# Kernel tuning notes

Hardware: AMD Instinct MI355X
Metric: run time of the kernel (lower is better)

The kernel has to match this reference:

```python
import math
import jax, jax.numpy as jnp
import numpy as np

NUM_HEADS = 8
EMBED_DIM = 512   # embed_dim_per_head(64) * num_heads(8)
LATENT = 256
HIDDEN = 512
INPUT_DIM = 128
P = 3             # function 'Q' -> 3 polynomial coefficients


def setup_inputs() -> dict:
    key = jax.random.key(0)
    ks = jax.random.split(key, 16)
    B, L, T, D, E = 64, 2048, 1024, INPUT_DIM, EMBED_DIM
    s = lambda fan_in: 1.0 / math.sqrt(fan_in)
    inp = {
        "timesteps": jax.random.uniform(ks[0], (B, L), jnp.float32),
        "X": jax.random.normal(ks[1], (B, L, D), jnp.float32),
        "M": jax.random.bernoulli(ks[2], 0.5, (B, L, D)).astype(jnp.float32),
        "y_time_steps": jax.random.uniform(ks[3], (B, T), jnp.float32),
        # time_embedding: Linear(1, E)
        "w_te": jax.random.normal(ks[4], (E,), jnp.float32),
        "b_te": jnp.zeros((E,), jnp.float32),
        # learned query [1, P, E]
        "query": jax.random.normal(ks[5], (1, P, E), jnp.float32),
        # query_map / key_map: Linear(E, E), stored [in, out]
        "W_q": jax.random.normal(ks[6], (E, E), jnp.float32) * s(E),
        "b_q": jnp.zeros((E,), jnp.float32),
        "W_k": jax.random.normal(ks[7], (E, E), jnp.float32) * s(E),
        "b_k": jnp.zeros((E,), jnp.float32),
        # attn out: Linear(2*D*H, latent)
        "W_o": jax.random.normal(ks[8], (2 * D * NUM_HEADS, LATENT), jnp.float32) * s(2 * D * NUM_HEADS),
        "b_o": jnp.zeros((LATENT,), jnp.float32),
        # decoder MLP: latent -> hidden -> hidden -> D
        "W1": jax.random.normal(ks[9], (LATENT, HIDDEN), jnp.float32) * s(LATENT),
        "b1": jnp.zeros((HIDDEN,), jnp.float32),
        "W2": jax.random.normal(ks[10], (HIDDEN, HIDDEN), jnp.float32) * s(HIDDEN),
        "b2": jnp.zeros((HIDDEN,), jnp.float32),
        "W3": jax.random.normal(ks[11], (HIDDEN, D), jnp.float32) * s(HIDDEN),
        "b3": jnp.zeros((D,), jnp.float32),
    }
    return inp


def _fld_forward(timesteps, X, M, y_time_steps, w_te, b_te, query,
                 W_q, b_q, W_k, b_k, W_o, b_o, W1, b1, W2, b2, W3, b3):
    B, L = timesteps.shape
    D = X.shape[-1]
    E, H = EMBED_DIM, NUM_HEADS
    ek = E // H
    # learn_time_embedding: Linear(1,E) then sin on indices range(0, E, H)
    key = timesteps[..., None] * w_te + b_te                      # [B,L,E]
    sin_mask = (jnp.arange(E) % H) == 0
    key = jnp.where(sin_mask, jnp.sin(key), key)
    Xcat = jnp.concatenate([X, M], axis=-1)                       # [B,L,2D]
    Mcat = jnp.concatenate([M, M], axis=-1)                       # [B,L,2D]
    # mask is used only for masked_fill in torch (no grad through it)
    maskb = jax.lax.stop_gradient((Mcat != 0).astype(Xcat.dtype))
    q = jnp.broadcast_to(query, (B, P, E)) @ W_q + b_q            # [B,P,E]
    k = key @ W_k + b_k                                            # [B,L,E]
    qh = q.reshape(B, P, H, ek).transpose(0, 2, 1, 3)             # [B,H,P,ek]
    kh = k.reshape(B, L, H, ek).transpose(0, 2, 1, 3)             # [B,H,L,ek]
    scores = jnp.einsum('bhpe,bhle->bhpl', qh, kh) / math.sqrt(ek)
    # per-channel masked softmax over L, factorized (masked entries -> exp(-1e9)=0)
    m = jnp.max(scores, axis=-1, keepdims=True)
    w = jnp.exp(scores - m)                                        # [B,H,P,L]
    num = jnp.einsum('bhpl,blc->bhpc', w, maskb * Xcat)            # [B,H,P,2D]
    den = jnp.einsum('bhpl,blc->bhpc', w, maskb)
    x = num / den                                                  # [B,H,P,2D]
    x = x.transpose(0, 2, 1, 3).reshape(B, P, H * 2 * D)
    coeffs = x @ W_o + b_o                                         # [B,P,latent]
    t = y_time_steps[..., None]                                    # [B,T,1]
    c0 = coeffs[:, 0:1, :]
    c1 = coeffs[:, 1:2, :]
    c2 = coeffs[:, 2:3, :]
    z = c0 + t * c1 + (t * t) * c2                                 # [B,T,latent]
    h1 = jax.nn.relu(z @ W1 + b1)
    h2 = jax.nn.relu(h1 @ W2 + b2)
    return h2 @ W3 + b3                                            # [B,T,D]


def reference(timesteps, X, M, y_time_steps, w_te, b_te, query,
              W_q, b_q, W_k, b_k, W_o, b_o, W1, b1, W2, b2, W3, b3):
    return _fld_forward(timesteps, X, M, y_time_steps, w_te, b_te, query,
                        W_q, b_q, W_k, b_k, W_o, b_o, W1, b1, W2, b2, W3, b3)
```

## Files before the change

### kernel.cpp

```cpp
#include <hip/hip_runtime.h>
#include <math.h>

#define NH   8
#define PP   3
#define HP   24
#define E    512
#define EK   64
#define D    128
#define LL   2048
#define BB   64
#define TT   1024
#define LAT  256
#define HID  512
#define CH   8
#define CL   256

typedef __attribute__((ext_vector_type(8))) short bf16x8;
typedef __attribute__((ext_vector_type(4))) float f32x4;
typedef __attribute__((ext_vector_type(16))) float f32x16;

#define OFF_VS     ((size_t)2048)
#define OFF_WA     ((size_t)4096)
#define OFF_WB     ((size_t)4128)
#define OFF_SB     ((size_t)4160)
#define OFF_CVP    ((size_t)73728)
#define OFF_P2     ((size_t)81920)
#define OFF_PART   ((size_t)475136)
#define OFF_SC     ((size_t)3620864)
#define OFF_A      ((size_t)3784704)

__device__ inline ushort f2bf(float x) {
    union { float f; uint u; } v; v.f = x;
    uint r = v.u + 0x7fffu + ((v.u >> 16) & 1u);
    return (ushort)(r >> 16);
}
__device__ inline uint swz(uint a)  { return a ^ (((a >> 8) & 7u) << 4); }
__device__ inline uint swzH(uint a) { return a ^ (((a >> 7) & 7u) << 4); }
__device__ inline uint swzQ(uint a) { return a ^ (((a >> 9) & 7u) << 4); }
__device__ inline uint pk2(float lo, float hi) {
    return (uint)f2bf(lo) | ((uint)f2bf(hi) << 16);
}
__device__ inline float h1f(float a0, float a1, float a2, float t) {
    return fmaxf(fmaf(t, fmaf(t, a2, a1), a0), 0.f);
}
__device__ inline int sigma(int s) { return s ^ (((((s >> 2) ^ (s >> 3)) & 1)) ? 12 : 0); }

__global__ __launch_bounds__(512) void k_setup(const float* __restrict__ query,
                                               const float* __restrict__ W_q,
                                               const float* __restrict__ b_q,
                                               const float* __restrict__ W_k,
                                               const float* __restrict__ b_k,
                                               const float* __restrict__ w_te,
                                               const float* __restrict__ b_te,
                                               const float* __restrict__ W_o,
                                               float* __restrict__ vsin,
                                               float* __restrict__ wA,
                                               float* __restrict__ wB,
                                               float* __restrict__ sbias,
                                               float* __restrict__ cvp) {
    int bx = blockIdx.x, tid = threadIdx.x;
    if (bx < HP) {
        int hp = bx, h = hp / PP, p = hp % PP;
        __shared__ float q_s[EK];
        if (tid < EK) {
            float acc = b_q[h * EK + tid];
            for (int i = 0; i < E; ++i)
                acc += query[p * E + i] * W_q[(size_t)i * E + h * EK + tid];
            q_s[tid] = acc;
        }
        __syncthreads();
        int e = tid;
        const float scale = 0.125f;
        float acc = 0.f;
        for (int j = 0; j < EK; ++j)
            acc += W_k[(size_t)e * E + h * EK + j] * q_s[j];
        float v = acc * scale;
        if ((e & 7) == 0) vsin[hp * 64 + (e >> 3)] = v;
        __shared__ float r1[512], r2[512];
        r1[e] = v * w_te[e];
        r2[e] = v * b_te[e];
        __syncthreads();
        for (int s = 256; s > 0; s >>= 1) {
            if (e < s) { r1[e] += r1[e + s]; r2[e] += r2[e + s]; }
            __syncthreads();
        }
        if (e == 0) {
            wA[hp] = r1[0];
            wB[hp] = r2[0];
            float sb = 0.f;
            for (int j = 0; j < EK; ++j) sb += b_k[h * EK + j] * q_s[j];
            sbias[hp] = sb * scale;
        }
    } else {
        int bc = bx - HP;
        int h = bc >> 2, cc = bc & 3, o = tid & 255;
        float acc = 0.f;
        #pragma unroll 8
        for (int c = cc * 32; c < cc * 32 + 32; ++c)
            acc += W_o[(size_t)(h * 256 + 128 + c) * LAT + o];
        cvp[(h * 4 + cc) * LAT + o] = acc;
    }
}

__global__ __launch_bounds__(512) void k_wsf(const float* __restrict__ timesteps,
                                             const float* __restrict__ w_te,
                                             const float* __restrict__ b_te,
                                             const float* __restrict__ vsin,
                                             const float* __restrict__ wA,
                                             const float* __restrict__ wB,
                                             const float* __restrict__ sb,
                                             const float* __restrict__ X,
                                             const float* __restrict__ M,
                                             float* __restrict__ part) {
    __shared__ float vs_s[HP * 64];
    __shared__ float w8_s[64], b8_s[64];
    __shared__ float wA_s[HP], wB_s[HP], sb_s[HP];
    __shared__ ushort w_s[32 * 256];
    __shared__ ushort vt[256 * 64];
    int b = blockIdx.x / CH, ch = blockIdx.x % CH;
    int l0 = ch * CL;
    int tid = threadIdx.x;

    for (int i = tid; i < HP * 64; i += 512) vs_s[i] = vsin[i];
    if (tid < 64) { w8_s[tid] = w_te[tid * 8]; b8_s[tid] = b_te[tid * 8]; }
    if (tid < HP) { wA_s[tid] = wA[tid]; wB_s[tid] = wB[tid]; sb_s[tid] = sb[tid]; }
    __syncthreads();

    {
        int lpair = tid & 127, hh = tid >> 7;
        float ts0 = timesteps[(size_t)b * LL + l0 + lpair * 2];
        float ts1 = timesteps[(size_t)b * LL + l0 + lpair * 2 + 1];
        float sc0[6], sc1[6];
        #pragma unroll
        for (int i = 0; i < 6; ++i) {
            int hp = hh * 6 + i;
            sc0[i] = fmaf(ts0, wA_s[hp], wB_s[hp]) + sb_s[hp];
            sc1[i] = fmaf(ts1, wA_s[hp], wB_s[hp]) + sb_s[hp];
        }
        for (int jc = 0; jc < 64; jc += 16) {
            float d0[16], d1[16];
            #pragma unroll
            for (int j = 0; j < 16; ++j) {
                float w = w8_s[jc + j], bb = b8_s[jc + j];
                float k0 = fmaf(ts0, w, bb), k1 = fmaf(ts1, w, bb);
                d0[j] = __sinf(k0) - k0;
                d1[j] = __sinf(k1) - k1;
            }
            #pragma unroll
            for (int i = 0; i < 6; ++i) {
                int hp = hh * 6 + i;
                #pragma unroll
                for (int j = 0; j < 16; j += 4) {
                    float4 v4 = *(const float4*)&vs_s[hp * 64 + jc + j];
                    sc0[i] += d0[j] * v4.x + d0[j+1] * v4.y + d0[j+2] * v4.z + d0[j+3] * v4.w;
                    sc1[i] += d1[j] * v4.x + d1[j+1] * v4.y + d1[j+2] * v4.z + d1[j+3] * v4.w;
                }
            }
        }
        #pragma unroll
        for (int i = 0; i < 6; ++i) {
            int hp = hh * 6 + i;
            *(uint*)((char*)w_s + swzQ((uint)(hp * 512 + lpair * 4))) = pk2(__expf(sc0[i]), __expf(sc1[i]));
        }
        for (int idx = tid; idx < 8 * 128; idx += 512) {
            int hp = 24 + (idx >> 7), lp = idx & 127;
            *(uint*)((char*)w_s + swzQ((uint)(hp * 512 + lp * 4))) = 0u;
        }
    }

    int lane = tid & 63, wv = tid >> 6;
    int l31 = lane & 31, hl = lane >> 5;
    f32x16 acc;
    #pragma unroll
    for (int e = 0; e < 16; ++e) acc[e] = 0.f;

    int cst = tid & 127, lg = tid >> 7;
    for (int q = 0; q < 4; ++q) {
        if (q) __syncthreads();
        #pragma unroll
        for (int i = 0; i < 8; ++i) {
            int ll = lg * 16 + i * 2;
            size_t g0 = ((size_t)b * LL + l0 + q * 64 + ll) * D + cst;
            float m0 = M[g0], m1 = M[g0 + D];
            float x0 = X[g0] * m0, x1 = X[g0 + D] * m1;
            *(uint*)((char*)vt + swzH((uint)(cst * 128 + ll * 2)))         = pk2(x0, x1);
            *(uint*)((char*)vt + swzH((uint)((128 + cst) * 128 + ll * 2))) = pk2(m0, m1);
        }
        __syncthreads();
        #pragma unroll
        for (int ks = 0; ks < 4; ++ks) {
            bf16x8 af = *(const bf16x8*)((char*)w_s + swzQ((uint)(l31 * 512 + (q * 64 + ks * 16 + hl * 8) * 2)));
            bf16x8 bf_ = *(const bf16x8*)((char*)vt + swzH((uint)((wv * 32 + l31) * 128 + (ks * 16 + hl * 8) * 2)));
            acc = __builtin_amdgcn_mfma_f32_32x32x16_bf16(af, bf_, acc, 0, 0, 0);
        }
    }
    size_t base = ((size_t)(b * CH + ch) * HP) * 256;
    #pragma unroll
    for (int reg = 0; reg < 12; ++reg) {
        int hp = (reg & 3) + 8 * (reg >> 2) + 4 * hl;
        part[base + (size_t)hp * 256 + wv * 32 + l31] = acc[reg];
    }
}

__global__ __launch_bounds__(512) void k_mid(const float* __restrict__ part,
                                             const float* __restrict__ W_o,
                                             float* __restrict__ part2,
                                             const float* __restrict__ W2,
                                             const float* __restrict__ W3,
                                             ushort* __restrict__ W2F,
                                             ushort* __restrict__ W3F) {
    int bx = blockIdx.x, tid = threadIdx.x;
    if (bx < BB * NH) {
        int b = bx >> 3, h = bx & 7, t = tid & 255;
        __shared__ float ratio[PP][D];
        for (int ii = t; ii < PP * D; ii += 256) {
            int p = ii >> 7, c = ii & 127;
            int hp = h * PP + p;
            float n = 0.f, d = 0.f;
            for (int ch = 0; ch < CH; ++ch) {
                size_t base = ((size_t)(b * CH + ch) * HP + hp) * 256;
                n += part[base + c];
                d += part[base + 128 + c];
            }
            ratio[p][c] = n / d;
        }
        __syncthreads();
        int o = t;
        float a0 = 0.f, a1 = 0.f, a2 = 0.f;
        #pragma unroll 4
        for (int c = 0; c < D; ++c) {
            float w = W_o[(size_t)(h * 256 + c) * LAT + o];
            a0 = fmaf(ratio[0][c], w, a0);
            a1 = fmaf(ratio[1][c], w, a1);
            a2 = fmaf(ratio[2][c], w, a2);
        }
        size_t base = (((size_t)b * NH + h) * PP) * LAT + o;
        part2[base]           = a0;
        part2[base + LAT]     = a1;
        part2[base + 2 * LAT] = a2;
    } else {
        int gid = (bx - BB * NH) * 512 + tid;
        int l = gid & 63;
        int kb = 8 * (l >> 5);
        int cb = l & 31;
        if (gid < 32768) {
            int F = gid >> 6;
            int JT = F & 15, ks = F >> 4;
            int cbp = sigma(cb);
            int k0 = ks * 16 + kb, j = JT * 32 + cbp;
            #pragma unroll
            for (int e = 0; e < 8; ++e)
                W2F[(size_t)gid * 8 + e] = f2bf(W2[(size_t)(k0 + e) * HID + j]);
        } else {
            int g2 = gid - 32768;
            int F2 = g2 >> 6;
            int CT = F2 & 3, KT = F2 >> 2;
            int k0 = KT * 16 + kb, c = CT * 32 + cb;
            #pragma unroll
            for (int e = 0; e < 8; ++e)
                W3F[(size_t)g2 * 8 + e] = f2bf(W3[(size_t)(k0 + e) * D + c]);
        }
    }
}

__global__ __launch_bounds__(512) void k_avec3p(const float* __restrict__ part2,
                                                const float* __restrict__ cvp,
                                                const float* __restrict__ b_o,
                                                const float* __restrict__ W1,
                                                const float* __restrict__ b1,
                                                float* __restrict__ abuf) {
    int b = blockIdx.x, tid = threadIdx.x;
    __shared__ float cf[PP * LAT];
    for (int idx = tid; idx < PP * LAT; idx += 512) {
        int p = idx / LAT, o = idx % LAT;
        float s = b_o[o];
        #pragma unroll 8
        for (int i = 0; i < 32; ++i) s += cvp[i * LAT + o];
        for (int h = 0; h < NH; ++h)
            s += part2[(((size_t)b * NH + h) * PP + p) * LAT + o];
        cf[p * LAT + o] = s;
    }
    __syncthreads();
    int j = tid;
    float a0 = b1[j], a1 = 0.f, a2 = 0.f;
    #pragma unroll 4
    for (int k = 0; k < LAT; ++k) {
        float w = W1[(size_t)k * HID + j];
        a0 = fmaf(cf[k], w, a0);
        a1 = fmaf(cf[LAT + k], w, a1);
        a2 = fmaf(cf[2 * LAT + k], w, a2);
    }
    abuf[(size_t)b * 3 * HID + j] = a0;
    abuf[(size_t)b * 3 * HID + HID + j] = a1;
    abuf[(size_t)b * 3 * HID + 2 * HID + j] = a2;
}

__global__ __launch_bounds__(512, 2) void k_mlp13(const float* __restrict__ abuf,
                                                  const float* __restrict__ yts,
                                                  const ushort* __restrict__ W2F,
                                                  const float* __restrict__ b2,
                                                  const ushort* __restrict__ W3F,
                                                  const float* __restrict__ b3,
                                                  float* __restrict__ out) {
    __shared__ char lds[65536];
    int b = blockIdx.x, t0 = blockIdx.y * 64, tid = threadIdx.x;
    const float* a0p = abuf + (size_t)b * 3 * HID;
    const float* a1p = a0p + HID;
    const float* a2p = a1p + HID;

    {
        int sr = tid & 63, sub0 = (tid >> 6) & 1, skp = tid >> 7;
        float t = yts[(size_t)b * TT + t0 + sr];
        int kg0 = skp * 128 + sub0 * 64;
        uint sbase = (uint)(skp * 16384 + sr * 256 + sub0 * 128);
        #pragma unroll
        for (int i = 0; i < 8; ++i) {
            int k = kg0 + i * 8;
            float4 xa0 = *(const float4*)(a0p + k), xb0 = *(const float4*)(a0p + k + 4);
            float4 xa1 = *(const float4*)(a1p + k), xb1 = *(const float4*)(a1p + k + 4);
            float4 xa2 = *(const float4*)(a2p + k), xb2 = *(const float4*)(a2p + k + 4);
            uint4 pk;
            pk.x = pk2(h1f(xa0.x, xa1.x, xa2.x, t), h1f(xa0.y, xa1.y, xa2.y, t));
            pk.y = pk2(h1f(xa0.z, xa1.z, xa2.z, t), h1f(xa0.w, xa1.w, xa2.w, t));
            pk.z = pk2(h1f(xb0.x, xb1.x, xb2.x, t), h1f(xb0.y, xb1.y, xb2.y, t));
            pk.w = pk2(h1f(xb0.z, xb1.z, xb2.z, t), h1f(xb0.w, xb1.w, xb2.w, t));
            *(uint4*)(lds + swz(sbase + i * 16)) = pk;
        }
    }
    __syncthreads();

    int lane = tid & 63, w = tid >> 6;
    int l31 = lane & 31, hl = lane >> 5;
    int wp = w & 1, gw = w >> 1;
    int Jb = gw * 4 + wp * 2;

    f32x16 acc[2][2];
    #pragma unroll
    for (int jt = 0; jt < 2; ++jt) {
        int jT = (Jb + jt) * 32;
        #pragma unroll
        for (int reg = 0; reg < 16; ++reg) {
            int slot = (reg & 3) + 8 * (reg >> 2) + 4 * hl;
            float bv = b2[jT + sigma(slot)];
            acc[jt][0][reg] = bv;
            acc[jt][1][reg] = bv;
        }
    }
    bf16x8 afA[2][2], afB[2][2];
    #pragma unroll
    for (int u = 0; u < 2; ++u)
        #pragma unroll
        for (int jt = 0; jt < 2; ++jt)
            afA[u][jt] = *(const bf16x8*)(W2F + ((size_t)(u * 16 + Jb + jt) * 64 + lane) * 8);
    #pragma unroll
    for (int g = 0; g < 16; ++g) {
        int ks0 = g * 2;
        if (g < 15) {
            #pragma unroll
            for (int u = 0; u < 2; ++u)
                #pragma unroll
                for (int jt = 0; jt < 2; ++jt) {
                    bf16x8 v = *(const bf16x8*)(W2F + ((size_t)((ks0 + 2 + u) * 16 + Jb + jt) * 64 + lane) * 8);
                    if (g & 1) afA[u][jt] = v; else afB[u][jt] = v;
                }
        }
        #pragma unroll
        for (int u = 0; u < 2; ++u) {
            int ks = ks0 + u;
            uint base = (uint)((ks >> 3) * 16384 + (ks & 7) * 32 + hl * 16);
            bf16x8 bh0 = *(const bf16x8*)(lds + swz(base + (uint)(l31 * 256)));
            bf16x8 bh1 = *(const bf16x8*)(lds + swz(base + (uint)((32 + l31) * 256)));
            #pragma unroll
            for (int jt = 0; jt < 2; ++jt) {
                bf16x8 af = (g & 1) ? afB[u][jt] : afA[u][jt];
                acc[jt][0] = __builtin_amdgcn_mfma_f32_32x32x16_bf16(af, bh0, acc[jt][0], 0, 0, 0);
                acc[jt][1] = __builtin_amdgcn_mfma_f32_32x32x16_bf16(af, bh1, acc[jt][1], 0, 0, 0);
            }
        }
    }
    __syncthreads();

    #pragma unroll
    for (int jt = 0; jt < 2; ++jt) {
        int J = Jb + jt;
        #pragma unroll
        for (int rtile = 0; rtile < 2; ++rtile)
            #pragma unroll
            for (int s = 0; s < 2; ++s) {
                uint4 uu;
                uu.x = pk2(fmaxf(acc[jt][rtile][8 * s + 0], 0.f), fmaxf(acc[jt][rtile][8 * s + 1], 0.f));
                uu.y = pk2(fmaxf(acc[jt][rtile][8 * s + 2], 0.f), fmaxf(acc[jt][rtile][8 * s + 3], 0.f));
                uu.z = pk2(fmaxf(acc[jt][rtile][8 * s + 4], 0.f), fmaxf(acc[jt][rtile][8 * s + 5], 0.f));
                uu.w = pk2(fmaxf(acc[jt][rtile][8 * s + 6], 0.f), fmaxf(acc[jt][rtile][8 * s + 7], 0.f));
                *(uint4*)(lds + (uint)((rtile * 32 + J * 2 + s) * 1024 + lane * 16)) = uu;
            }
    }
    __syncthreads();

    f32x16 acc2a, acc2b;
    {
        float bv = b3[gw * 32 + l31];
        #pragma unroll
        for (int e = 0; e < 16; ++e) { acc2a[e] = bv; acc2b[e] = 0.f; }
    }
    bf16x8 bwA[4], bwB[4];
    #pragma unroll
    for (int u = 0; u < 4; ++u)
        bwA[u] = *(const bf16x8*)(W3F + ((size_t)(u * 4 + gw) * 64 + lane) * 8);
    #pragma unroll
    for (int g = 0; g < 8; ++g) {
        int sg0 = g * 4;
        if (g < 7) {
            #pragma unroll
            for (int u = 0; u < 4; ++u) {
                bf16x8 v = *(const bf16x8*)(W3F + ((size_t)((sg0 + 4 + u) * 4 + gw) * 64 + lane) * 8);
                if (g & 1) bwA[u] = v; else bwB[u] = v;
            }
        }
        #pragma unroll
        for (int u = 0; u < 4; ++u) {
            bf16x8 ah = *(const bf16x8*)(lds + (uint)((wp * 32 + sg0 + u) * 1024 + lane * 16));
            bf16x8 bw = (g & 1) ? bwB[u] : bwA[u];
            if (u & 1)
                acc2b = __builtin_amdgcn_mfma_f32_32x32x16_bf16(ah, bw, acc2b, 0, 0, 0);
            else
                acc2a = __builtin_amdgcn_mfma_f32_32x32x16_bf16(ah, bw, acc2a, 0, 0, 0);
        }
    }

    {
        int c = gw * 32 + l31;
        size_t rowbase = (size_t)b * TT + t0 + wp * 32 + 4 * hl;
        #pragma unroll
        for (int reg = 0; reg < 16; ++reg)
            out[(rowbase + (reg & 3) + 8 * (reg >> 2)) * D + c] = acc2a[reg] + acc2b[reg];
    }
}

extern "C" void kernel_launch(void* const* d_in, const int* in_sizes, int n_in,
                              void* d_out, int out_size, void* d_ws, size_t ws_size,
                              hipStream_t stream) {
    const float* timesteps = (const float*)d_in[0];
    const float* X        = (const float*)d_in[1];
    const float* M        = (const float*)d_in[2];
    const float* yts      = (const float*)d_in[3];
    const float* w_te     = (const float*)d_in[4];
    const float* b_te     = (const float*)d_in[5];
    const float* query    = (const float*)d_in[6];
    const float* W_q      = (const float*)d_in[7];
    const float* b_q      = (const float*)d_in[8];
    const float* W_k      = (const float*)d_in[9];
    const float* b_k      = (const float*)d_in[10];
    const float* W_o      = (const float*)d_in[11];
    const float* b_o      = (const float*)d_in[12];
    const float* W1       = (const float*)d_in[13];
    const float* b1       = (const float*)d_in[14];
    const float* W2       = (const float*)d_in[15];
    const float* b2       = (const float*)d_in[16];
    const float* W3       = (const float*)d_in[17];
    const float* b3       = (const float*)d_in[18];
    float* out = (float*)d_out;
    float* ws  = (float*)d_ws;

    float* vsin   = ws + OFF_VS;
    float* wA     = ws + OFF_WA;
    float* wB     = ws + OFF_WB;
    float* sbias  = ws + OFF_SB;
    float* cvp    = ws + OFF_CVP;
    float* part2  = ws + OFF_P2;
    float* part   = ws + OFF_PART;
    float* abuf   = ws + OFF_A;
    ushort* W2F   = (ushort*)(ws + OFF_SC);
    ushort* W3F   = W2F + (size_t)HID * HID;

    hipLaunchKernelGGL(k_setup,  dim3(HP + 32),       dim3(512), 0, stream,
                       query, W_q, b_q, W_k, b_k, w_te, b_te, W_o, vsin, wA, wB, sbias, cvp);
    hipLaunchKernelGGL(k_wsf,    dim3(BB * CH),       dim3(512), 0, stream,
                       timesteps, w_te, b_te, vsin, wA, wB, sbias, X, M, part);
    hipLaunchKernelGGL(k_mid,    dim3(BB * NH + 80),  dim3(512), 0, stream,
                       part, W_o, part2, W2, W3, W2F, W3F);
    hipLaunchKernelGGL(k_avec3p, dim3(BB),            dim3(512), 0, stream,
                       part2, cvp, b_o, W1, b1, abuf);
    hipLaunchKernelGGL(k_mlp13,  dim3(BB, TT / 64),   dim3(512), 0, stream,
                       abuf, yts, W2F, b2, W3F, b3, out);
}
```

Baseline: 149.8 us.

## Stream W2/W3 MFMA fragments into LDS via double-buffered direct global-to-LDS loads

```diff
diff --git a/kernel.cpp b/kernel.cpp
--- a/kernel.cpp
+++ b/kernel.cpp
@@ -44,6 +44,9 @@
     return fmaxf(fmaf(t, fmaf(t, a2, a1), a0), 0.f);
 }
 __device__ inline int sigma(int s) { return s ^ (((((s >> 2) ^ (s >> 3)) & 1)) ? 12 : 0); }
+
+#define WAITV4 { asm volatile("s_waitcnt vmcnt(4)" ::: "memory"); __builtin_amdgcn_sched_barrier(0); }
+#define WAITV0 { asm volatile("s_waitcnt vmcnt(0)" ::: "memory"); __builtin_amdgcn_sched_barrier(0); }
 
 __global__ __launch_bounds__(512) void k_setup(const float* __restrict__ query,
                                                const float* __restrict__ W_q,
@@ -295,14 +298,14 @@
     abuf[(size_t)b * 3 * HID + 2 * HID + j] = a2;
 }
 
-__global__ __launch_bounds__(512, 2) void k_mlp13(const float* __restrict__ abuf,
+__global__ __launch_bounds__(512, 2) void k_mlp14(const float* __restrict__ abuf,
                                                   const float* __restrict__ yts,
                                                   const ushort* __restrict__ W2F,
                                                   const float* __restrict__ b2,
                                                   const ushort* __restrict__ W3F,
                                                   const float* __restrict__ b3,
                                                   float* __restrict__ out) {
-    __shared__ char lds[65536];
+    __shared__ char lds[131072];
     int b = blockIdx.x, t0 = blockIdx.y * 64, tid = threadIdx.x;
     const float* a0p = abuf + (size_t)b * 3 * HID;
     const float* a1p = a0p + HID;
@@ -333,6 +336,7 @@
     int l31 = lane & 31, hl = lane >> 5;
     int wp = w & 1, gw = w >> 1;
     int Jb = gw * 4 + wp * 2;
+    uint wbase = 65536u + (uint)w * 8192u;
 
     f32x16 acc[2][2];
     #pragma unroll
@@ -346,36 +350,44 @@
             acc[jt][1][reg] = bv;
         }
     }
-    bf16x8 afA[2][2], afB[2][2];
-    #pragma unroll
-    for (int u = 0; u < 2; ++u)
-        #pragma unroll
-        for (int jt = 0; jt < 2; ++jt)
-            afA[u][jt] = *(const bf16x8*)(W2F + ((size_t)(u * 16 + Jb + jt) * 64 + lane) * 8);
+    WAITV0;
+    #pragma unroll
+    for (int g = 0; g < 2; ++g)
+        #pragma unroll
+        for (int u = 0; u < 2; ++u)
+            #pragma unroll
+            for (int jt = 0; jt < 2; ++jt) {
+                const ushort* gp = W2F + (((size_t)(g * 2 + u) * 16 + Jb + jt) * 64 + lane) * 8;
+                __builtin_amdgcn_global_load_lds((const uint*)gp,
+                    (uint*)(lds + wbase + (uint)g * 4096u + (uint)(u * 2 + jt) * 1024u), 16, 0, 0);
+            }
     #pragma unroll
     for (int g = 0; g < 16; ++g) {
-        int ks0 = g * 2;
-        if (g < 15) {
+        if (g == 15) WAITV0 else WAITV4;
+        uint pbuf = wbase + (uint)(g & 1) * 4096u;
+        #pragma unroll
+        for (int u = 0; u < 2; ++u) {
+            int ks = g * 2 + u;
+            uint hbase = (uint)((ks >> 3) * 16384 + (ks & 7) * 32 + hl * 16);
+            bf16x8 bh0 = *(const bf16x8*)(lds + swz(hbase + (uint)(l31 * 256)));
+            bf16x8 bh1 = *(const bf16x8*)(lds + swz(hbase + (uint)((32 + l31) * 256)));
+            #pragma unroll
+            for (int jt = 0; jt < 2; ++jt) {
+                bf16x8 af = *(const bf16x8*)(lds + pbuf + (uint)(u * 2 + jt) * 1024u + (uint)lane * 16u);
+                acc[jt][0] = __builtin_amdgcn_mfma_f32_32x32x16_bf16(af, bh0, acc[jt][0], 0, 0, 0);
+                acc[jt][1] = __builtin_amdgcn_mfma_f32_32x32x16_bf16(af, bh1, acc[jt][1], 0, 0, 0);
+            }
+        }
+        if (g < 14) {
+            __builtin_amdgcn_sched_barrier(0);
             #pragma unroll
             for (int u = 0; u < 2; ++u)
                 #pragma unroll
                 for (int jt = 0; jt < 2; ++jt) {
-                    bf16x8 v = *(const bf16x8*)(W2F + ((size_t)((ks0 + 2 + u) * 16 + Jb + jt) * 64 + lane) * 8);
-                    if (g & 1) afA[u][jt] = v; else afB[u][jt] = v;
+                    const ushort* gp = W2F + (((size_t)((g + 2) * 2 + u) * 16 + Jb + jt) * 64 + lane) * 8;
+                    __builtin_amdgcn_global_load_lds((const uint*)gp,
+                        (uint*)(lds + wbase + (uint)(g & 1) * 4096u + (uint)(u * 2 + jt) * 1024u), 16, 0, 0);
                 }
-        }
-        #pragma unroll
-        for (int u = 0; u < 2; ++u) {
-            int ks = ks0 + u;
-            uint base = (uint)((ks >> 3) * 16384 + (ks & 7) * 32 + hl * 16);
-            bf16x8 bh0 = *(const bf16x8*)(lds + swz(base + (uint)(l31 * 256)));
-            bf16x8 bh1 = *(const bf16x8*)(lds + swz(base + (uint)((32 + l31) * 256)));
-            #pragma unroll
-            for (int jt = 0; jt < 2; ++jt) {
-                bf16x8 af = (g & 1) ? afB[u][jt] : afA[u][jt];
-                acc[jt][0] = __builtin_amdgcn_mfma_f32_32x32x16_bf16(af, bh0, acc[jt][0], 0, 0, 0);
-                acc[jt][1] = __builtin_amdgcn_mfma_f32_32x32x16_bf16(af, bh1, acc[jt][1], 0, 0, 0);
-            }
         }
     }
     __syncthreads();
@@ -403,28 +415,37 @@
         #pragma unroll
         for (int e = 0; e < 16; ++e) { acc2a[e] = bv; acc2b[e] = 0.f; }
     }
-    bf16x8 bwA[4], bwB[4];
-    #pragma unroll
-    for (int u = 0; u < 4; ++u)
-        bwA[u] = *(const bf16x8*)(W3F + ((size_t)(u * 4 + gw) * 64 + lane) * 8);
+    WAITV0;
+    #pragma unroll
+    for (int g = 0; g < 2; ++g)
+        #pragma unroll
+        for (int u = 0; u < 4; ++u) {
+            const ushort* gp = W3F + (((size_t)(g * 4 + u) * 4 + gw) * 64 + lane) * 8;
+            __builtin_amdgcn_global_load_lds((const uint*)gp,
+                (uint*)(lds + wbase + (uint)g * 4096u + (uint)u * 1024u), 16, 0, 0);
+        }
     #pragma unroll
     for (int g = 0; g < 8; ++g) {
-        int sg0 = g * 4;
-        if (g < 7) {
-            #pragma unroll
-            for (int u = 0; u < 4; ++u) {
-                bf16x8 v = *(const bf16x8*)(W3F + ((size_t)((sg0 + 4 + u) * 4 + gw) * 64 + lane) * 8);
-                if (g & 1) bwA[u] = v; else bwB[u] = v;
-            }
-        }
+        if (g == 7) WAITV0 else WAITV4;
+        uint pbuf = wbase + (uint)(g & 1) * 4096u;
         #pragma unroll
         for (int u = 0; u < 4; ++u) {
-            bf16x8 ah = *(const bf16x8*)(lds + (uint)((wp * 32 + sg0 + u) * 1024 + lane * 16));
-            bf16x8 bw = (g & 1) ? bwB[u] : bwA[u];
+            int sg = g * 4 + u;
+            bf16x8 ah = *(const bf16x8*)(lds + (uint)((wp * 32 + sg) * 1024 + lane * 16));
+            bf16x8 bw = *(const bf16x8*)(lds + pbuf + (uint)u * 1024u + (uint)lane * 16u);
             if (u & 1)
                 acc2b = __builtin_amdgcn_mfma_f32_32x32x16_bf16(ah, bw, acc2b, 0, 0, 0);
             else
                 acc2a = __builtin_amdgcn_mfma_f32_32x32x16_bf16(ah, bw, acc2a, 0, 0, 0);
+        }
+        if (g < 6) {
+            __builtin_amdgcn_sched_barrier(0);
+            #pragma unroll
+            for (int u = 0; u < 4; ++u) {
+                const ushort* gp = W3F + (((size_t)((g + 2) * 4 + u) * 4 + gw) * 64 + lane) * 8;
+                __builtin_amdgcn_global_load_lds((const uint*)gp,
+                    (uint*)(lds + wbase + (uint)(g & 1) * 4096u + (uint)u * 1024u), 16, 0, 0);
+            }
         }
     }
 
@@ -481,6 +502,6 @@
                        part, W_o, part2, W2, W3, W2F, W3F);
     hipLaunchKernelGGL(k_avec3p, dim3(BB),            dim3(512), 0, stream,
                        part2, cvp, b_o, W1, b1, abuf);
-    hipLaunchKernelGGL(k_mlp13,  dim3(BB, TT / 64),   dim3(512), 0, stream,
+    hipLaunchKernelGGL(k_mlp14,  dim3(BB, TT / 64),   dim3(512), 0, stream,
                        abuf, yts, W2F, b2, W3F, b3, out);
 }
```

Measured after the change: 158.1 us. 1.06x slower.
